# Kernel optimization log

Measured on AMD Instinct MI355X. Metric: run time of the kernel, lower is better.

Reference implementation:

```python
import jax, jax.numpy as jnp
import numpy as np

B, N, D = 32, 128, 64
E = N * N
EPS = 1e-5


def _bn(x, gamma, beta):
    # torch BatchNorm1d on (B, C, D): normalize per-channel over (batch, last dim)
    mean = jnp.mean(x, axis=(0, 2), keepdims=True)
    var = jnp.var(x, axis=(0, 2), keepdims=True)
    return (x - mean) * jax.lax.rsqrt(var + EPS) * gamma[None, :, None] + beta[None, :, None]


def _gat_layer(x, edge, Wh, We, Wp, Wa, gv, bv, ge, be):
    b, n, d = x.shape
    res = x
    z_h = jnp.einsum('bnd,od->bno', x, Wh)   # fc_h (torch Linear: y = x W^T)
    z_e = jnp.einsum('bed,od->beo', edge, We)  # fc_e
    # incidence matmuls are pure gathers: edge e = i*n + j
    z_src = jnp.broadcast_to(z_h[:, None, :, :], (b, n, n, d)).reshape(b, n * n, d)  # start: edge (i,j) <- node j
    z_dst = jnp.broadcast_to(z_h[:, :, None, :], (b, n, n, d)).reshape(b, n * n, d)  # end:   edge (i,j) <- node i
    z = jnp.concatenate([z_src, z_dst, z_e], axis=-1)  # (b, E, 3d)
    z_e_new = jnp.einsum('bec,oc->beo', z, Wp)  # fc_proj
    attn = jnp.einsum('bec,c->be', z, Wa[0])    # attn_fc -> (b, E)
    attn = jnp.where(attn >= 0, attn, 0.01 * attn)  # LeakyReLU(0.01)
    attn = jax.nn.softmax(attn.reshape(b, n, n), axis=2).reshape(b, n * n)  # softmax over sources j
    # scatter via end^T: node i <- sum_j attn[i,j] * z_src[i*n+j]
    agg = (attn[:, :, None] * z_src).reshape(b, n, n, d).sum(axis=2)
    x_new = jax.nn.elu(res + _bn(agg, gv, bv))
    edge_new = jax.nn.elu(_bn(z_e_new, ge, be))
    return x_new, edge_new


def setup_inputs():
    key = jax.random.key(0)
    ks = jax.random.split(key, 10)
    scale = float(np.sqrt(2.0 / D))
    return {
        'x': jax.random.normal(ks[0], (B, N, D), jnp.float32),
        'edge': jax.random.normal(ks[1], (B, E, D), jnp.float32),
        'Wh1': jax.random.normal(ks[2], (D, D), jnp.float32) * scale,
        'We1': jax.random.normal(ks[3], (D, D), jnp.float32) * scale,
        'Wp1': jax.random.normal(ks[4], (D, 3 * D), jnp.float32) * scale,
        'Wa1': jax.random.normal(ks[5], (1, 3 * D), jnp.float32) * scale,
        'Wh2': jax.random.normal(ks[6], (D, D), jnp.float32) * scale,
        'We2': jax.random.normal(ks[7], (D, D), jnp.float32) * scale,
        'Wp2': jax.random.normal(ks[8], (D, 3 * D), jnp.float32) * scale,
        'Wa2': jax.random.normal(ks[9], (1, 3 * D), jnp.float32) * scale,
        'gv1': jnp.ones((N,), jnp.float32), 'bv1': jnp.zeros((N,), jnp.float32),
        'ge1': jnp.ones((E,), jnp.float32), 'be1': jnp.zeros((E,), jnp.float32),
        'gv2': jnp.ones((N,), jnp.float32), 'bv2': jnp.zeros((N,), jnp.float32),
        'ge2': jnp.ones((E,), jnp.float32), 'be2': jnp.zeros((E,), jnp.float32),
    }


def reference(x, edge, Wh1, We1, Wp1, Wa1, Wh2, We2, Wp2, Wa2,
              gv1, bv1, ge1, be1, gv2, bv2, ge2, be2):
    x, edge = _gat_layer(x, edge, Wh1, We1, Wp1, Wa1, gv1, bv1, ge1, be1)
    x, edge = _gat_layer(x, edge, Wh2, We2, Wp2, Wa2, gv2, bv2, ge2, be2)
    return x, edge
```

## Files before the change

kernel.cpp:

```cpp
#include <hip/hip_runtime.h>
#include <math.h>

#define BB 32
#define NN 128
#define DD 64
#define EE (NN*NN)
#define EPSI 1e-5f

typedef __attribute__((ext_vector_type(8))) short bf16x8;
typedef __attribute__((ext_vector_type(4))) float f32x4;

__device__ __forceinline__ short f2bf(float f) {
    union { float f; unsigned u; } v; v.f = f;
    unsigned u = v.u;
    unsigned r = (u + 0x7FFFu + ((u >> 16) & 1u)) >> 16;
    return (short)r;
}
__device__ __forceinline__ float dot4(float4 a, float4 b) {
    return a.x*b.x + a.y*b.y + a.z*b.z + a.w*b.w;
}
__device__ __forceinline__ float elu(float v) {
    return v > 0.f ? v : __expf(v) - 1.f;
}

__global__ void k_fold(const float* __restrict__ Wp, const float* __restrict__ We,
                       const float* __restrict__ Wa,
                       short* __restrict__ Mbf, float* __restrict__ w)
{
    int t = blockIdx.x * 256 + threadIdx.x;
    int d = t >> 6, k = t & 63;
    float acc = 0.f;
    for (int o = 0; o < DD; ++o)
        acc += Wp[d*192 + 128 + o] * We[o*DD + k];
    Mbf[d*DD + k] = f2bf(acc);
    if (d == 0) {
        float aw = 0.f;
        for (int o = 0; o < DD; ++o)
            aw += Wa[128 + o] * We[o*DD + k];
        w[k] = aw;
    }
}

__global__ void k_node(const float* __restrict__ x, const float* __restrict__ Wh,
                       const float* __restrict__ Wp, const float* __restrict__ Wa,
                       float* __restrict__ zh, float* __restrict__ Ps,
                       float* __restrict__ Pd, float* __restrict__ sO,
                       float* __restrict__ tO)
{
    int row = blockIdx.x;
    int d = threadIdx.x;
    __shared__ float xr[DD];
    __shared__ float zr[DD];
    xr[d] = x[row*DD + d];
    __syncthreads();
    float acc = 0.f;
#pragma unroll
    for (int k = 0; k < DD; ++k) acc += xr[k] * Wh[d*DD + k];
    zr[d] = acc;
    zh[row*DD + d] = acc;
    __syncthreads();
    float a0 = 0.f, a1 = 0.f;
#pragma unroll
    for (int o = 0; o < DD; ++o) {
        float z = zr[o];
        a0 += Wp[d*192 + o]      * z;
        a1 += Wp[d*192 + 64 + o] * z;
    }
    Ps[row*DD + d] = a0;
    Pd[row*DD + d] = a1;
    float sv = zr[d] * Wa[d];
    float tv = zr[d] * Wa[64 + d];
#pragma unroll
    for (int off = 32; off; off >>= 1) {
        sv += __shfl_xor(sv, off);
        tv += __shfl_xor(tv, off);
    }
    if (d == 0) { sO[row] = sv; tO[row] = tv; }
}

__global__ __launch_bounds__(64, 4) void k_edge(
    const float* __restrict__ ein,
    const short* __restrict__ Mbf,
    const float* __restrict__ wvec,
    const float* __restrict__ Ps,
    const float* __restrict__ Pd,
    const float* __restrict__ ge, const float* __restrict__ be,
    float* __restrict__ eout, float* __restrict__ uout)
{
    __shared__ float zl[32][68];

    const int l  = threadIdx.x;
    const int lr = l & 15;
    const int lg = l >> 4;
    const int e  = blockIdx.x;
    const int i0 = e >> 7, j0 = e & 127;

    bf16x8 bfr[4][2];
#pragma unroll
    for (int n = 0; n < 4; ++n)
#pragma unroll
        for (int s = 0; s < 2; ++s)
            bfr[n][s] = *reinterpret_cast<const bf16x8*>(Mbf + (16*n + lr)*DD + s*32 + lg*8);
    float4 wlo[2], whi[2];
#pragma unroll
    for (int s = 0; s < 2; ++s) {
        wlo[s] = *reinterpret_cast<const float4*>(wvec + s*32 + lg*8);
        whi[s] = *reinterpret_cast<const float4*>(wvec + s*32 + lg*8 + 4);
    }

    f32x4 acc[2][4];
#pragma unroll
    for (int m = 0; m < 2; ++m)
#pragma unroll
        for (int n = 0; n < 4; ++n)
            acc[m][n] = (f32x4){0.f, 0.f, 0.f, 0.f};

#pragma unroll
    for (int m = 0; m < 2; ++m) {
        const int b = 16*m + lr;
        const float* rowp = ein + ((size_t)b*EE + e)*DD;
        const float4 a0lo = *reinterpret_cast<const float4*>(rowp +      lg*8);
        const float4 a0hi = *reinterpret_cast<const float4*>(rowp +      lg*8 + 4);
        const float4 a1lo = *reinterpret_cast<const float4*>(rowp + 32 + lg*8);
        const float4 a1hi = *reinterpret_cast<const float4*>(rowp + 32 + lg*8 + 4);
        float up = dot4(a0lo, wlo[0]) + dot4(a0hi, whi[0])
                 + dot4(a1lo, wlo[1]) + dot4(a1hi, whi[1]);
        up += __shfl_xor(up, 16);
        up += __shfl_xor(up, 32);
        if (lg == 0) uout[(size_t)b*EE + e] = up;
        bf16x8 a0, a1;
        a0[0]=f2bf(a0lo.x); a0[1]=f2bf(a0lo.y); a0[2]=f2bf(a0lo.z); a0[3]=f2bf(a0lo.w);
        a0[4]=f2bf(a0hi.x); a0[5]=f2bf(a0hi.y); a0[6]=f2bf(a0hi.z); a0[7]=f2bf(a0hi.w);
        a1[0]=f2bf(a1lo.x); a1[1]=f2bf(a1lo.y); a1[2]=f2bf(a1lo.z); a1[3]=f2bf(a1lo.w);
        a1[4]=f2bf(a1hi.x); a1[5]=f2bf(a1hi.y); a1[6]=f2bf(a1hi.z); a1[7]=f2bf(a1hi.w);
#pragma unroll
        for (int n = 0; n < 4; ++n) {
            acc[m][n] = __builtin_amdgcn_mfma_f32_16x16x32_bf16(a0, bfr[n][0], acc[m][n], 0, 0, 0);
            acc[m][n] = __builtin_amdgcn_mfma_f32_16x16x32_bf16(a1, bfr[n][1], acc[m][n], 0, 0, 0);
        }
    }

#pragma unroll
    for (int m = 0; m < 2; ++m)
#pragma unroll
        for (int n = 0; n < 4; ++n)
#pragma unroll
            for (int q = 0; q < 4; ++q)
                zl[16*m + 4*lg + q][16*n + lr] = acc[m][n][q];
    __syncthreads();

    const int q4 = lr*4;
    float s1 = 0.f, s2 = 0.f;
#pragma unroll
    for (int it = 0; it < 8; ++it) {
        const int b = lg + 4*it;
        float4 z = *reinterpret_cast<float4*>(&zl[b][q4]);
        const float4 ps = *reinterpret_cast<const float4*>(Ps + (b*NN + j0)*DD + q4);
        const float4 pd = *reinterpret_cast<const float4*>(Pd + (b*NN + i0)*DD + q4);
        z.x += ps.x + pd.x; z.y += ps.y + pd.y;
        z.z += ps.z + pd.z; z.w += ps.w + pd.w;
        s1 += z.x + z.y + z.z + z.w;
        s2 += z.x*z.x + z.y*z.y + z.z*z.z + z.w*z.w;
        *reinterpret_cast<float4*>(&zl[b][q4]) = z;
    }
#pragma unroll
    for (int off = 1; off < 64; off <<= 1) {
        s1 += __shfl_xor(s1, off);
        s2 += __shfl_xor(s2, off);
    }
    const float mean  = s1 * (1.f/2048.f);
    const float var   = s2 * (1.f/2048.f) - mean*mean;
    const float sc = ge[e] * rsqrtf(var + EPSI);
    const float sh = be[e] - mean*sc;
    __syncthreads();

#pragma unroll
    for (int it = 0; it < 8; ++it) {
        const int b = lg + 4*it;
        float4 z = *reinterpret_cast<float4*>(&zl[b][q4]);
        z.x = elu(z.x*sc + sh);
        z.y = elu(z.y*sc + sh);
        z.z = elu(z.z*sc + sh);
        z.w = elu(z.w*sc + sh);
        *reinterpret_cast<float4*>(eout + ((size_t)b*EE + e)*DD + q4) = z;
    }
}

__global__ void k_attn(const float* __restrict__ sI, const float* __restrict__ tI,
                       const float* __restrict__ u, const float* __restrict__ zh,
                       float* __restrict__ agg)
{
    int blk = blockIdx.x; int b = blk >> 7, i = blk & 127;
    int l = threadIdx.x;
    __shared__ float at[NN];
    float ti = tI[blk];
    float l0 = sI[b*NN + l]      + ti + u[b*EE + i*NN + l];
    float l1 = sI[b*NN + l + 64] + ti + u[b*EE + i*NN + l + 64];
    l0 = l0 >= 0.f ? l0 : 0.01f*l0;
    l1 = l1 >= 0.f ? l1 : 0.01f*l1;
    float mx = fmaxf(l0, l1);
#pragma unroll
    for (int off = 32; off; off >>= 1) mx = fmaxf(mx, __shfl_xor(mx, off));
    float e0 = __expf(l0 - mx), e1 = __expf(l1 - mx);
    float sm = e0 + e1;
#pragma unroll
    for (int off = 32; off; off >>= 1) sm += __shfl_xor(sm, off);
    float inv = 1.f / sm;
    at[l]      = e0 * inv;
    at[l + 64] = e1 * inv;
    __syncthreads();
    float acc = 0.f;
    for (int j = 0; j < NN; ++j) acc += at[j] * zh[(b*NN + j)*DD + l];
    agg[(b*NN + i)*DD + l] = acc;
}

__global__ void k_vbn(const float* __restrict__ agg, const float* __restrict__ xres,
                      const float* __restrict__ gv, const float* __restrict__ bv,
                      float* __restrict__ xout)
{
    int i = blockIdx.x, t = threadIdx.x;
    float vals[8];
    float s1 = 0.f, s2 = 0.f;
#pragma unroll
    for (int q = 0; q < 8; ++q) {
        int m = t + 256*q; int b = m >> 6, d = m & 63;
        float v = agg[(b*NN + i)*DD + d];
        vals[q] = v; s1 += v; s2 += v*v;
    }
#pragma unroll
    for (int off = 1; off < 64; off <<= 1) {
        s1 += __shfl_xor(s1, off);
        s2 += __shfl_xor(s2, off);
    }
    __shared__ float r1[4], r2[4];
    int wv = t >> 6;
    if ((t & 63) == 0) { r1[wv] = s1; r2[wv] = s2; }
    __syncthreads();
    s1 = r1[0] + r1[1] + r1[2] + r1[3];
    s2 = r2[0] + r2[1] + r2[2] + r2[3];
    float mean  = s1 * (1.f/2048.f);
    float var   = s2 * (1.f/2048.f) - mean*mean;
    float scale = gv[i] * rsqrtf(var + EPSI);
    float shift = bv[i] - mean*scale;
#pragma unroll
    for (int q = 0; q < 8; ++q) {
        int m = t + 256*q; int b = m >> 6, d = m & 63;
        float v = vals[q]*scale + shift + xres[(b*NN + i)*DD + d];
        xout[(b*NN + i)*DD + d] = v > 0.f ? v : __expf(v) - 1.f;
    }
}

extern "C" void kernel_launch(void* const* d_in, const int* in_sizes, int n_in,
                              void* d_out, int out_size, void* d_ws, size_t ws_size,
                              hipStream_t stream)
{
    const float* x    = (const float*)d_in[0];
    const float* edge = (const float*)d_in[1];
    const float* Wh1  = (const float*)d_in[2];
    const float* We1  = (const float*)d_in[3];
    const float* Wp1  = (const float*)d_in[4];
    const float* Wa1  = (const float*)d_in[5];
    const float* Wh2  = (const float*)d_in[6];
    const float* We2  = (const float*)d_in[7];
    const float* Wp2  = (const float*)d_in[8];
    const float* Wa2  = (const float*)d_in[9];
    const float* gv1  = (const float*)d_in[10];
    const float* bv1  = (const float*)d_in[11];
    const float* ge1  = (const float*)d_in[12];
    const float* be1  = (const float*)d_in[13];
    const float* gv2  = (const float*)d_in[14];
    const float* bv2  = (const float*)d_in[15];
    const float* ge2  = (const float*)d_in[16];
    const float* be2  = (const float*)d_in[17];

    float* xout = (float*)d_out;
    float* eout = (float*)d_out + BB*NN*DD;

    float* ws  = (float*)d_ws;
    short* Mbf = (short*)ws;  ws += DD*DD/2;
    float* wv  = ws;  ws += DD;
    float* zh  = ws;  ws += BB*NN*DD;
    float* Ps  = ws;  ws += BB*NN*DD;
    float* Pd  = ws;  ws += BB*NN*DD;
    float* sb  = ws;  ws += BB*NN;
    float* tb  = ws;  ws += BB*NN;
    float* ub  = ws;  ws += BB*EE;
    float* agg = ws;  ws += BB*NN*DD;
    float* x1  = ws;  ws += BB*NN*DD;

    k_fold<<<16, 256, 0, stream>>>(Wp1, We1, Wa1, Mbf, wv);
    k_node<<<BB*NN, 64, 0, stream>>>(x, Wh1, Wp1, Wa1, zh, Ps, Pd, sb, tb);
    k_edge<<<EE, 64, 0, stream>>>(edge, Mbf, wv, Ps, Pd, ge1, be1, eout, ub);
    k_attn<<<BB*NN, 64, 0, stream>>>(sb, tb, ub, zh, agg);
    k_vbn<<<NN, 256, 0, stream>>>(agg, x, gv1, bv1, x1);
    k_fold<<<16, 256, 0, stream>>>(Wp2, We2, Wa2, Mbf, wv);
    k_node<<<BB*NN, 64, 0, stream>>>(x1, Wh2, Wp2, Wa2, zh, Ps, Pd, sb, tb);
    k_edge<<<EE, 64, 0, stream>>>(eout, Mbf, wv, Ps, Pd, ge2, be2, eout, ub);
    k_attn<<<BB*NN, 64, 0, stream>>>(sb, tb, ub, zh, agg);
    k_vbn<<<NN, 256, 0, stream>>>(agg, x1, gv2, bv2, xout);
}
```

Baseline: 224.7 us.

## Restructure edge kernel: drop LDS staging, fold attention dot into MFMA, 4 waves/block

The edge kernel now keeps the MFMA accumulators in registers. It seeds them with the Ps+Pd node projections and computes the batch-norm statistics and ELU output straight from those registers, which removes the shared-memory round trip and both barriers. The edge-attention dot product moves onto an extra MFMA using a bf16 weight fragment that is nonzero only in one column. Four edges are packed per 256-thread block, and the loads of the edge rows are issued up front. Output stores become scalar, strided by 16 floats per lane instead of float4, and the attention logit now has bf16 precision.

```diff
diff --git a/kernel.cpp b/kernel.cpp
--- a/kernel.cpp
+++ b/kernel.cpp
@@ -16,16 +16,13 @@
     unsigned r = (u + 0x7FFFu + ((u >> 16) & 1u)) >> 16;
     return (short)r;
 }
-__device__ __forceinline__ float dot4(float4 a, float4 b) {
-    return a.x*b.x + a.y*b.y + a.z*b.z + a.w*b.w;
-}
 __device__ __forceinline__ float elu(float v) {
     return v > 0.f ? v : __expf(v) - 1.f;
 }
 
 __global__ void k_fold(const float* __restrict__ Wp, const float* __restrict__ We,
                        const float* __restrict__ Wa,
-                       short* __restrict__ Mbf, float* __restrict__ w)
+                       short* __restrict__ Mbf, short* __restrict__ wbf)
 {
     int t = blockIdx.x * 256 + threadIdx.x;
     int d = t >> 6, k = t & 63;
@@ -37,7 +34,7 @@
         float aw = 0.f;
         for (int o = 0; o < DD; ++o)
             aw += Wa[128 + o] * We[o*DD + k];
-        w[k] = aw;
+        wbf[k] = f2bf(aw);
     }
 }
 
@@ -78,22 +75,31 @@
     if (d == 0) { sO[row] = sv; tO[row] = tv; }
 }
 
-__global__ __launch_bounds__(64, 4) void k_edge(
+__global__ __launch_bounds__(256, 4) void k_edge(
     const float* __restrict__ ein,
     const short* __restrict__ Mbf,
-    const float* __restrict__ wvec,
+    const short* __restrict__ wbf,
     const float* __restrict__ Ps,
     const float* __restrict__ Pd,
     const float* __restrict__ ge, const float* __restrict__ be,
     float* __restrict__ eout, float* __restrict__ uout)
 {
-    __shared__ float zl[32][68];
-
-    const int l  = threadIdx.x;
+    const int l  = threadIdx.x & 63;
+    const int wv = threadIdx.x >> 6;
     const int lr = l & 15;
     const int lg = l >> 4;
-    const int e  = blockIdx.x;
+    const int e  = blockIdx.x * 4 + wv;
     const int i0 = e >> 7, j0 = e & 127;
+
+    float4 ald[2][4];
+#pragma unroll
+    for (int m = 0; m < 2; ++m) {
+        const float* rowp = ein + ((size_t)(16*m + lr)*EE + e)*DD;
+        ald[m][0] = *reinterpret_cast<const float4*>(rowp +      lg*8);
+        ald[m][1] = *reinterpret_cast<const float4*>(rowp +      lg*8 + 4);
+        ald[m][2] = *reinterpret_cast<const float4*>(rowp + 32 + lg*8);
+        ald[m][3] = *reinterpret_cast<const float4*>(rowp + 32 + lg*8 + 4);
+    }
 
     bf16x8 bfr[4][2];
 #pragma unroll
@@ -101,88 +107,78 @@
 #pragma unroll
         for (int s = 0; s < 2; ++s)
             bfr[n][s] = *reinterpret_cast<const bf16x8*>(Mbf + (16*n + lr)*DD + s*32 + lg*8);
-    float4 wlo[2], whi[2];
-#pragma unroll
-    for (int s = 0; s < 2; ++s) {
-        wlo[s] = *reinterpret_cast<const float4*>(wvec + s*32 + lg*8);
-        whi[s] = *reinterpret_cast<const float4*>(wvec + s*32 + lg*8 + 4);
-    }
+    const bf16x8 zerov = (bf16x8){0,0,0,0,0,0,0,0};
+    bf16x8 wfrag[2];
+#pragma unroll
+    for (int s = 0; s < 2; ++s)
+        wfrag[s] = (lr == 0) ? *reinterpret_cast<const bf16x8*>(wbf + s*32 + lg*8) : zerov;
 
     f32x4 acc[2][4];
+    f32x4 uacc[2];
+#pragma unroll
+    for (int m = 0; m < 2; ++m) {
+        uacc[m] = (f32x4){0.f, 0.f, 0.f, 0.f};
+#pragma unroll
+        for (int q = 0; q < 4; ++q) {
+            const int b = 16*m + 4*lg + q;
+            const float* ps = Ps + ((size_t)(b*NN + j0))*DD + lr;
+            const float* pd = Pd + ((size_t)(b*NN + i0))*DD + lr;
+#pragma unroll
+            for (int n = 0; n < 4; ++n)
+                acc[m][n][q] = ps[16*n] + pd[16*n];
+        }
+    }
+
+#pragma unroll
+    for (int m = 0; m < 2; ++m) {
+        bf16x8 a0, a1;
+        a0[0]=f2bf(ald[m][0].x); a0[1]=f2bf(ald[m][0].y); a0[2]=f2bf(ald[m][0].z); a0[3]=f2bf(ald[m][0].w);
+        a0[4]=f2bf(ald[m][1].x); a0[5]=f2bf(ald[m][1].y); a0[6]=f2bf(ald[m][1].z); a0[7]=f2bf(ald[m][1].w);
+        a1[0]=f2bf(ald[m][2].x); a1[1]=f2bf(ald[m][2].y); a1[2]=f2bf(ald[m][2].z); a1[3]=f2bf(ald[m][2].w);
+        a1[4]=f2bf(ald[m][3].x); a1[5]=f2bf(ald[m][3].y); a1[6]=f2bf(ald[m][3].z); a1[7]=f2bf(ald[m][3].w);
+#pragma unroll
+        for (int n = 0; n < 4; ++n)
+            acc[m][n] = __builtin_amdgcn_mfma_f32_16x16x32_bf16(a0, bfr[n][0], acc[m][n], 0, 0, 0);
+        uacc[m] = __builtin_amdgcn_mfma_f32_16x16x32_bf16(a0, wfrag[0], uacc[m], 0, 0, 0);
+#pragma unroll
+        for (int n = 0; n < 4; ++n)
+            acc[m][n] = __builtin_amdgcn_mfma_f32_16x16x32_bf16(a1, bfr[n][1], acc[m][n], 0, 0, 0);
+        uacc[m] = __builtin_amdgcn_mfma_f32_16x16x32_bf16(a1, wfrag[1], uacc[m], 0, 0, 0);
+    }
+
+    float s1 = 0.f, s2 = 0.f;
 #pragma unroll
     for (int m = 0; m < 2; ++m)
 #pragma unroll
         for (int n = 0; n < 4; ++n)
-            acc[m][n] = (f32x4){0.f, 0.f, 0.f, 0.f};
-
-#pragma unroll
-    for (int m = 0; m < 2; ++m) {
-        const int b = 16*m + lr;
-        const float* rowp = ein + ((size_t)b*EE + e)*DD;
-        const float4 a0lo = *reinterpret_cast<const float4*>(rowp +      lg*8);
-        const float4 a0hi = *reinterpret_cast<const float4*>(rowp +      lg*8 + 4);
-        const float4 a1lo = *reinterpret_cast<const float4*>(rowp + 32 + lg*8);
-        const float4 a1hi = *reinterpret_cast<const float4*>(rowp + 32 + lg*8 + 4);
-        float up = dot4(a0lo, wlo[0]) + dot4(a0hi, whi[0])
-                 + dot4(a1lo, wlo[1]) + dot4(a1hi, whi[1]);
-        up += __shfl_xor(up, 16);
-        up += __shfl_xor(up, 32);
-        if (lg == 0) uout[(size_t)b*EE + e] = up;
-        bf16x8 a0, a1;
-        a0[0]=f2bf(a0lo.x); a0[1]=f2bf(a0lo.y); a0[2]=f2bf(a0lo.z); a0[3]=f2bf(a0lo.w);
-        a0[4]=f2bf(a0hi.x); a0[5]=f2bf(a0hi.y); a0[6]=f2bf(a0hi.z); a0[7]=f2bf(a0hi.w);
-        a1[0]=f2bf(a1lo.x); a1[1]=f2bf(a1lo.y); a1[2]=f2bf(a1lo.z); a1[3]=f2bf(a1lo.w);
-        a1[4]=f2bf(a1hi.x); a1[5]=f2bf(a1hi.y); a1[6]=f2bf(a1hi.z); a1[7]=f2bf(a1hi.w);
-#pragma unroll
-        for (int n = 0; n < 4; ++n) {
-            acc[m][n] = __builtin_amdgcn_mfma_f32_16x16x32_bf16(a0, bfr[n][0], acc[m][n], 0, 0, 0);
-            acc[m][n] = __builtin_amdgcn_mfma_f32_16x16x32_bf16(a1, bfr[n][1], acc[m][n], 0, 0, 0);
-        }
-    }
-
-#pragma unroll
-    for (int m = 0; m < 2; ++m)
-#pragma unroll
-        for (int n = 0; n < 4; ++n)
-#pragma unroll
-            for (int q = 0; q < 4; ++q)
-                zl[16*m + 4*lg + q][16*n + lr] = acc[m][n][q];
-    __syncthreads();
-
-    const int q4 = lr*4;
-    float s1 = 0.f, s2 = 0.f;
-#pragma unroll
-    for (int it = 0; it < 8; ++it) {
-        const int b = lg + 4*it;
-        float4 z = *reinterpret_cast<float4*>(&zl[b][q4]);
-        const float4 ps = *reinterpret_cast<const float4*>(Ps + (b*NN + j0)*DD + q4);
-        const float4 pd = *reinterpret_cast<const float4*>(Pd + (b*NN + i0)*DD + q4);
-        z.x += ps.x + pd.x; z.y += ps.y + pd.y;
-        z.z += ps.z + pd.z; z.w += ps.w + pd.w;
-        s1 += z.x + z.y + z.z + z.w;
-        s2 += z.x*z.x + z.y*z.y + z.z*z.z + z.w*z.w;
-        *reinterpret_cast<float4*>(&zl[b][q4]) = z;
-    }
+#pragma unroll
+            for (int q = 0; q < 4; ++q) { float v = acc[m][n][q]; s1 += v; s2 += v*v; }
 #pragma unroll
     for (int off = 1; off < 64; off <<= 1) {
         s1 += __shfl_xor(s1, off);
         s2 += __shfl_xor(s2, off);
     }
-    const float mean  = s1 * (1.f/2048.f);
-    const float var   = s2 * (1.f/2048.f) - mean*mean;
+    const float mean = s1 * (1.f/2048.f);
+    const float var  = s2 * (1.f/2048.f) - mean*mean;
     const float sc = ge[e] * rsqrtf(var + EPSI);
     const float sh = be[e] - mean*sc;
-    __syncthreads();
-
-#pragma unroll
-    for (int it = 0; it < 8; ++it) {
-        const int b = lg + 4*it;
-        float4 z = *reinterpret_cast<float4*>(&zl[b][q4]);
-        z.x = elu(z.x*sc + sh);
-        z.y = elu(z.y*sc + sh);
-        z.z = elu(z.z*sc + sh);
-        z.w = elu(z.w*sc + sh);
-        *reinterpret_cast<float4*>(eout + ((size_t)b*EE + e)*DD + q4) = z;
+
+#pragma unroll
+    for (int m = 0; m < 2; ++m)
+#pragma unroll
+        for (int q = 0; q < 4; ++q) {
+            const int b = 16*m + 4*lg + q;
+            float* orow = eout + ((size_t)b*EE + e)*DD + lr;
+#pragma unroll
+            for (int n = 0; n < 4; ++n)
+                orow[16*n] = elu(acc[m][n][q]*sc + sh);
+        }
+    if (lr == 0) {
+#pragma unroll
+        for (int m = 0; m < 2; ++m)
+#pragma unroll
+            for (int q = 0; q < 4; ++q)
+                uout[(size_t)(16*m + 4*lg + q)*EE + e] = uacc[m][q];
     }
 }
 
@@ -278,7 +274,7 @@
 
     float* ws  = (float*)d_ws;
     short* Mbf = (short*)ws;  ws += DD*DD/2;
-    float* wv  = ws;  ws += DD;
+    short* wbf = (short*)ws;  ws += DD/2;
     float* zh  = ws;  ws += BB*NN*DD;
     float* Ps  = ws;  ws += BB*NN*DD;
     float* Pd  = ws;  ws += BB*NN*DD;
@@ -288,14 +284,14 @@
     float* agg = ws;  ws += BB*NN*DD;
     float* x1  = ws;  ws += BB*NN*DD;
 
-    k_fold<<<16, 256, 0, stream>>>(Wp1, We1, Wa1, Mbf, wv);
+    k_fold<<<16, 256, 0, stream>>>(Wp1, We1, Wa1, Mbf, wbf);
     k_node<<<BB*NN, 64, 0, stream>>>(x, Wh1, Wp1, Wa1, zh, Ps, Pd, sb, tb);
-    k_edge<<<EE, 64, 0, stream>>>(edge, Mbf, wv, Ps, Pd, ge1, be1, eout, ub);
+    k_edge<<<EE/4, 256, 0, stream>>>(edge, Mbf, wbf, Ps, Pd, ge1, be1, eout, ub);
     k_attn<<<BB*NN, 64, 0, stream>>>(sb, tb, ub, zh, agg);
     k_vbn<<<NN, 256, 0, stream>>>(agg, x, gv1, bv1, x1);
-    k_fold<<<16, 256, 0, stream>>>(Wp2, We2, Wa2, Mbf, wv);
+    k_fold<<<16, 256, 0, stream>>>(Wp2, We2, Wa2, Mbf, wbf);
     k_node<<<BB*NN, 64, 0, stream>>>(x1, Wh2, Wp2, Wa2, zh, Ps, Pd, sb, tb);
-    k_edge<<<EE, 64, 0, stream>>>(eout, Mbf, wv, Ps, Pd, ge2, be2, eout, ub);
+    k_edge<<<EE/4, 256, 0, stream>>>(eout, Mbf, wbf, Ps, Pd, ge2, be2, eout, ub);
     k_attn<<<BB*NN, 64, 0, stream>>>(sb, tb, ub, zh, agg);
     k_vbn<<<NN, 256, 0, stream>>>(agg, x1, gv2, bv2, xout);
 }
```

After: 272.5 us. 21.3% more time.
